# Optimization experiments

Measured on AMD Instinct MI355X. Metric: run time of the kernel, lower is better.

The kernel has to match this reference:

```python
import jax, jax.numpy as jnp
import numpy as np
import math

N_NODES = 50000
N_EDGES = 800000
NFEAT = 512
NHID = 128
NCLASS = 128
NLAYERS = 16
LAMDA = 0.5
ALPHA = 0.1


def setup_inputs() -> dict:
    key = jax.random.key(0)
    k1, k2, k3, k4, k5, k6, k7, k8 = jax.random.split(key, 8)
    x = jax.random.normal(k1, (N_NODES, NFEAT), dtype=jnp.float32)
    # edges with no self loops: col = (row + offset) % N, offset in [1, N)
    row = jax.random.randint(k2, (N_EDGES,), 0, N_NODES, dtype=jnp.int32)
    off = jax.random.randint(k3, (N_EDGES,), 1, N_NODES, dtype=jnp.int32)
    col = (row + off) % N_NODES
    edge_idx = jnp.stack([row, col], axis=0)
    # conv weights: uniform(-stdv, stdv), stdv = 1/sqrt(out_features)
    stdv = 1.0 / math.sqrt(NHID)
    conv_w = jax.random.uniform(k4, (NLAYERS, NHID, NHID), jnp.float32, -stdv, stdv)
    # fc layers (stored as [in, out]; equivalent to torch Linear y = x @ W.T + b)
    fc0_w = jax.random.normal(k5, (NFEAT, NHID), jnp.float32) * (1.0 / math.sqrt(NFEAT))
    fc0_b = jax.random.normal(k6, (NHID,), jnp.float32) * 0.01
    fc1_w = jax.random.normal(k7, (NHID, NCLASS), jnp.float32) * (1.0 / math.sqrt(NHID))
    fc1_b = jax.random.normal(k8, (NCLASS,), jnp.float32) * 0.01
    return {"x": x, "edge_idx": edge_idx, "conv_w": conv_w,
            "fc0_w": fc0_w, "fc0_b": fc0_b, "fc1_w": fc1_w, "fc1_b": fc1_b}


def reference(x, edge_idx, conv_w, fc0_w, fc0_b, fc1_w, fc1_b):
    # eval mode: dropout is identity
    n = x.shape[0]
    loop = jnp.arange(n, dtype=edge_idx.dtype)
    # add_remaining_self_loops: inputs have no self loops -> append unit loops
    row = jnp.concatenate([edge_idx[0], loop])
    col = jnp.concatenate([edge_idx[1], loop])
    w = jnp.ones(row.shape[0], dtype=x.dtype)
    # symmetric normalization: D^-1/2 A D^-1/2
    deg = jax.ops.segment_sum(w, row, num_segments=n)
    dinv = jnp.where(deg > 0, jax.lax.rsqrt(deg), 0.0).astype(x.dtype)
    w = dinv[row] * w * dinv[col]

    h0 = jax.nn.relu(x @ fc0_w + fc0_b)  # [N, NHID]
    thetas = jnp.log(LAMDA / jnp.arange(1, NLAYERS + 1, dtype=x.dtype) + 1.0)

    def layer(h, wt):
        Wl, theta = wt
        # SpMM: hi[r] = sum_{(r,c) in E} w_rc * h[c]
        hi = jax.ops.segment_sum(w[:, None] * h[col], row, num_segments=n)
        support = (1.0 - ALPHA) * hi + ALPHA * h0
        out = theta * (support @ Wl) + (1.0 - theta) * support
        return jax.nn.relu(out), None

    h, _ = jax.lax.scan(layer, h0, (conv_w, thetas))
    return h @ fc1_w + fc1_b  # [N, NCLASS]
```

## Files before the change

### kernel.cpp

```cpp
#include <hip/hip_runtime.h>
#include <hip/hip_bf16.h>
#include <math.h>

#define N_NODES_C 50000
#define N_EDGES_C 800000
#define NFEAT_C 512
#define NH_C 128
#define NLAYERS_C 16
#define LDB 136

typedef __attribute__((ext_vector_type(8))) short short8;
typedef __attribute__((ext_vector_type(4))) float f32x4;

__device__ __forceinline__ float b2f(unsigned short h) {
    union { unsigned int u; float f; } v; v.u = ((unsigned int)h) << 16; return v.f;
}
__device__ __forceinline__ unsigned short f2b(float f) {
    union { float f; unsigned int u; } v; v.f = f;
    unsigned int r = (v.u + 0x7fffu + ((v.u >> 16) & 1u)) >> 16;
    return (unsigned short)r;
}


__global__ __launch_bounds__(256) void k_count(const int* __restrict__ row,
                                               int* __restrict__ cnt) {
    int e = blockIdx.x * 256 + threadIdx.x;
    atomicAdd(&cnt[row[e]], 1);
}

__global__ __launch_bounds__(256) void k_scan1(const int* __restrict__ cnt,
                                               int* __restrict__ locex,
                                               int* __restrict__ partials, int n) {
    __shared__ int sm[256];
    int t = threadIdx.x;
    int i = blockIdx.x * 256 + t;
    int v = (i < n) ? cnt[i] : 0;
    sm[t] = v;
    __syncthreads();
    for (int o = 1; o < 256; o <<= 1) {
        int x = (t >= o) ? sm[t - o] : 0;
        __syncthreads();
        sm[t] += x;
        __syncthreads();
    }
    if (i < n) locex[i] = sm[t] - v;
    if (t == 255) partials[blockIdx.x] = sm[255];
}

__global__ __launch_bounds__(256) void k_scan2(int* __restrict__ partials, int np) {
    __shared__ int sm[256];
    int t = threadIdx.x;
    int v = (t < np) ? partials[t] : 0;
    sm[t] = v;
    __syncthreads();
    for (int o = 1; o < 256; o <<= 1) {
        int x = (t >= o) ? sm[t - o] : 0;
        __syncthreads();
        sm[t] += x;
        __syncthreads();
    }
    if (t < np) partials[t] = sm[t] - v;
}

__global__ __launch_bounds__(256) void k_scan3(const int* __restrict__ cnt,
                                               const int* __restrict__ locex,
                                               const int* __restrict__ partials,
                                               int* __restrict__ rowptr,
                                               int* __restrict__ cursor,
                                               float* __restrict__ dinv,
                                               int n, int ne) {
    int i = blockIdx.x * 256 + threadIdx.x;
    if (i < n) {
        int rp = locex[i] + partials[i >> 8];
        rowptr[i] = rp;
        cursor[i] = rp;
        dinv[i] = 1.0f / sqrtf((float)(cnt[i] + 1));
    }
    if (i == 0) rowptr[n] = ne;
}

__global__ __launch_bounds__(256) void k_fill(const int* __restrict__ row,
                                              const int* __restrict__ col,
                                              int* __restrict__ cursor,
                                              int* __restrict__ colsorted) {
    int e = blockIdx.x * 256 + threadIdx.x;
    int p = atomicAdd(&cursor[row[e]], 1);
    colsorted[p] = col[e];
}


__global__ __launch_bounds__(256) void k_convt128(const float* __restrict__ src,
                                                  unsigned short* __restrict__ dst,
                                                  int total) {
    int i = blockIdx.x * 256 + threadIdx.x;
    if (i >= total) return;
    int l = i >> 14, w = i & 16383;
    int n = w >> 7, k = w & 127;
    dst[i] = f2b(src[(l << 14) + (k << 7) + n]);
}

__global__ __launch_bounds__(256) void k_convt_fc0(const float* __restrict__ src,
                                                   unsigned short* __restrict__ dst) {
    int i = blockIdx.x * 256 + threadIdx.x;
    int n = i >> 9, k = i & 511;
    dst[i] = f2b(src[(k << 7) + n]);
}


__device__ __forceinline__ void acc8(float* a, uint4 u) {
    a[0] += b2f((unsigned short)(u.x & 0xffffu));
    a[1] += b2f((unsigned short)(u.x >> 16));
    a[2] += b2f((unsigned short)(u.y & 0xffffu));
    a[3] += b2f((unsigned short)(u.y >> 16));
    a[4] += b2f((unsigned short)(u.z & 0xffffu));
    a[5] += b2f((unsigned short)(u.z >> 16));
    a[6] += b2f((unsigned short)(u.w & 0xffffu));
    a[7] += b2f((unsigned short)(u.w >> 16));
}

__global__ __launch_bounds__(256) void k_spmm(const unsigned short* __restrict__ hs,
                                              const unsigned short* __restrict__ h0,
                                              const float* __restrict__ dinv,
                                              const int* __restrict__ rowptr,
                                              const int* __restrict__ cols,
                                              unsigned short* __restrict__ sout) {
    const int w = threadIdx.x >> 6, ln = threadIdx.x & 63;
    const int r = blockIdx.x * 4 + w;
    const int g = ln >> 4, gi = ln & 15;
    const uint4* hs4 = (const uint4*)hs;
    const uint4* h04 = (const uint4*)h0;

    float a[8];
#pragma unroll
    for (int j = 0; j < 8; j++) a[j] = 0.f;

    int e = rowptr[r];
    const int end = rowptr[r + 1];

    if (g == 0) {
        uint4 u = hs4[(size_t)r * 16 + gi];
        acc8(a, u);
    }
    for (; e + 15 < end; e += 16) {
        int cA = cols[e + g];
        int cB = cols[e + 4 + g];
        int cC = cols[e + 8 + g];
        int cD = cols[e + 12 + g];
        uint4 uA = hs4[(size_t)cA * 16 + gi];
        uint4 uB = hs4[(size_t)cB * 16 + gi];
        uint4 uC = hs4[(size_t)cC * 16 + gi];
        uint4 uD = hs4[(size_t)cD * 16 + gi];
        acc8(a, uA);
        acc8(a, uB);
        acc8(a, uC);
        acc8(a, uD);
    }
    for (; e + 3 < end; e += 4) {
        int c = cols[e + g];
        uint4 u = hs4[(size_t)c * 16 + gi];
        acc8(a, u);
    }
    int rem = end - e;
    if (g < rem) {
        int c = cols[e + g];
        uint4 u = hs4[(size_t)c * 16 + gi];
        acc8(a, u);
    }

#pragma unroll
    for (int j = 0; j < 8; j++) {
        a[j] += __shfl_xor(a[j], 16);
        a[j] += __shfl_xor(a[j], 32);
    }

    float dr = 0.9f * dinv[r];
    uint4 hv = h04[(size_t)r * 16 + gi];
    uint4 o;
    o.x = (unsigned int)f2b(dr * a[0] + 0.1f * b2f((unsigned short)(hv.x & 0xffffu))) |
          ((unsigned int)f2b(dr * a[1] + 0.1f * b2f((unsigned short)(hv.x >> 16))) << 16);
    o.y = (unsigned int)f2b(dr * a[2] + 0.1f * b2f((unsigned short)(hv.y & 0xffffu))) |
          ((unsigned int)f2b(dr * a[3] + 0.1f * b2f((unsigned short)(hv.y >> 16))) << 16);
    o.z = (unsigned int)f2b(dr * a[4] + 0.1f * b2f((unsigned short)(hv.z & 0xffffu))) |
          ((unsigned int)f2b(dr * a[5] + 0.1f * b2f((unsigned short)(hv.z >> 16))) << 16);
    o.w = (unsigned int)f2b(dr * a[6] + 0.1f * b2f((unsigned short)(hv.w & 0xffffu))) |
          ((unsigned int)f2b(dr * a[7] + 0.1f * b2f((unsigned short)(hv.w >> 16))) << 16);
    if (g == 0) ((uint4*)sout)[(size_t)r * 16 + gi] = o;
}


__global__ __launch_bounds__(256) void k_gemm_blend(
    const unsigned short* __restrict__ S, const float* __restrict__ dinv,
    const unsigned short* __restrict__ WT, unsigned short* __restrict__ hdst,
    float theta, int use_dinv) {
    __shared__ __align__(16) unsigned short s_lds[64 * LDB];
    __shared__ __align__(16) unsigned short bt[128 * LDB];
    const int tid = threadIdx.x;
    const int w = tid >> 6, ln = tid & 63;
    const int quad = ln >> 4, l16 = ln & 15;
    const int block_base = blockIdx.x * 64;

    for (int chunk = tid; chunk < 128 * 16; chunk += 256) {
        int n = chunk >> 4, k8 = (chunk & 15) << 3;
        *(short8*)&bt[n * LDB + k8] = *(const short8*)&WT[(n << 7) + k8];
    }
    for (int chunk = tid; chunk < 64 * 16; chunk += 256) {
        int n = chunk >> 4, k8 = (chunk & 15) << 3;
        int row = block_base + n;
        short8 v = {};
        if (row < N_NODES_C) v = *(const short8*)&S[(size_t)row * NH_C + k8];
        *(short8*)&s_lds[n * LDB + k8] = v;
    }
    __syncthreads();

    f32x4 acc[8];
#pragma unroll
    for (int j = 0; j < 8; j++) acc[j] = (f32x4){0.f, 0.f, 0.f, 0.f};
#pragma unroll
    for (int ki = 0; ki < 128; ki += 32) {
        short8 af = *(const short8*)&s_lds[((w << 4) + l16) * LDB + ki + quad * 8];
#pragma unroll
        for (int nt = 0; nt < 8; nt++) {
            short8 bf = *(const short8*)&bt[(nt * 16 + l16) * LDB + ki + quad * 8];
            acc[nt] = __builtin_amdgcn_mfma_f32_16x16x32_bf16(af, bf, acc[nt], 0, 0, 0);
        }
    }

#pragma unroll
    for (int reg = 0; reg < 4; reg++) {
        int lr = (w << 4) + (quad << 2) + reg;
        int r = block_base + lr;
        float drv = dinv[(r < N_NODES_C) ? r : (N_NODES_C - 1)];
#pragma unroll
        for (int nt = 0; nt < 8; nt++) {
            int n = nt * 16 + l16;
            float s = b2f(s_lds[lr * LDB + n]);
            float v = theta * acc[nt][reg] + (1.f - theta) * s;
            v = fmaxf(v, 0.f);
            if (use_dinv) v *= drv;
            s_lds[lr * LDB + n] = f2b(v);
        }
    }
#pragma unroll
    for (int it = 0; it < 4; it++) {
        int local = ln + it * 64;
        int lr = (w << 4) + (local >> 4);
        int c8 = (local & 15) << 3;
        int row = block_base + lr;
        if (row < N_NODES_C)
            *(short8*)&hdst[(size_t)row * NH_C + c8] = *(const short8*)&s_lds[lr * LDB + c8];
    }
}


template <int AFP32, int MT>
__global__ __launch_bounds__(256) void k_gemm(
    const void* __restrict__ Av, const unsigned short* __restrict__ WT,
    int M, int K,
    const float* __restrict__ bias, const float* __restrict__ dinv,
    unsigned short* __restrict__ out0, unsigned short* __restrict__ out1,
    float* __restrict__ outf, int mode) {
    __shared__ __align__(16) unsigned short bt[128 * LDB];
    const int tid = threadIdx.x;
    const int w = tid >> 6, ln = tid & 63;
    const int quad = ln >> 4, l16 = ln & 15;
    const int ROWS = 64 * MT;
    const int block_base = blockIdx.x * ROWS;
    const int m_base = block_base + w * (16 * MT);

    f32x4 acc[MT][8];
#pragma unroll
    for (int i = 0; i < MT; i++)
#pragma unroll
        for (int j = 0; j < 8; j++) acc[i][j] = (f32x4){0.f, 0.f, 0.f, 0.f};

    for (int kc = 0; kc < K; kc += 128) {
        float4 a_f[MT][4][2];
        short8 a_b[MT][4];
#pragma unroll
        for (int ki4 = 0; ki4 < 4; ki4++) {
#pragma unroll
            for (int mt = 0; mt < MT; mt++) {
                int row = m_base + mt * 16 + l16;
                if (row >= M) row = M - 1;
                if (AFP32) {
                    const float* A = (const float*)Av;
                    const float* p = &A[(size_t)row * K + kc + ki4 * 32 + quad * 8];
                    a_f[mt][ki4][0] = *(const float4*)p;
                    a_f[mt][ki4][1] = *(const float4*)(p + 4);
                } else {
                    const unsigned short* A = (const unsigned short*)Av;
                    a_b[mt][ki4] =
                        *(const short8*)&A[(size_t)row * K + kc + ki4 * 32 + quad * 8];
                }
            }
        }
        for (int chunk = tid; chunk < 128 * 16; chunk += 256) {
            int n = chunk >> 4, k8 = (chunk & 15) << 3;
            *(short8*)&bt[n * LDB + k8] = *(const short8*)&WT[(size_t)n * K + kc + k8];
        }
        __syncthreads();
#pragma unroll
        for (int ki4 = 0; ki4 < 4; ki4++) {
            short8 bf[8];
#pragma unroll
            for (int nt = 0; nt < 8; nt++)
                bf[nt] = *(const short8*)&bt[(nt * 16 + l16) * LDB + ki4 * 32 + quad * 8];
#pragma unroll
            for (int mt = 0; mt < MT; mt++) {
                short8 af;
                if (AFP32) {
                    float4 f0 = a_f[mt][ki4][0];
                    float4 f1 = a_f[mt][ki4][1];
                    af[0] = (short)f2b(f0.x); af[1] = (short)f2b(f0.y);
                    af[2] = (short)f2b(f0.z); af[3] = (short)f2b(f0.w);
                    af[4] = (short)f2b(f1.x); af[5] = (short)f2b(f1.y);
                    af[6] = (short)f2b(f1.z); af[7] = (short)f2b(f1.w);
                } else {
                    af = a_b[mt][ki4];
                }
#pragma unroll
                for (int nt = 0; nt < 8; nt++)
                    acc[mt][nt] = __builtin_amdgcn_mfma_f32_16x16x32_bf16(
                        af, bf[nt], acc[mt][nt], 0, 0, 0);
            }
        }
        __syncthreads();
    }

    if (mode == 2) {
#pragma unroll
        for (int mt = 0; mt < MT; mt++)
#pragma unroll
            for (int reg = 0; reg < 4; reg++) {
                int r = m_base + mt * 16 + quad * 4 + reg;
                if (r >= M) continue;
#pragma unroll
                for (int nt = 0; nt < 8; nt++) {
                    int n = nt * 16 + l16;
                    outf[(size_t)r * NH_C + n] = acc[mt][nt][reg] + bias[n];
                }
            }
        return;
    }

#pragma unroll
    for (int mt = 0; mt < MT; mt++)
#pragma unroll
        for (int reg = 0; reg < 4; reg++) {
            int lr = w * (16 * MT) + mt * 16 + quad * 4 + reg;
#pragma unroll
            for (int nt = 0; nt < 8; nt++) {
                int n = nt * 16 + l16;
                float v = acc[mt][nt][reg] + bias[n];
                bt[lr * LDB + n] = f2b(fmaxf(v, 0.f));
            }
        }
#pragma unroll
    for (int it = 0; it < 4 * MT; it++) {
        int local = ln + it * 64;
        int lr = w * (16 * MT) + (local >> 4);
        int c8 = (local & 15) << 3;
        int row = block_base + lr;
        if (row >= M) continue;
        short8 v = *(const short8*)&bt[lr * LDB + c8];
        *(short8*)&out1[(size_t)row * NH_C + c8] = v;
        float dr = dinv[row];
        short8 o;
#pragma unroll
        for (int j = 0; j < 8; j++)
            o[j] = (short)f2b(b2f((unsigned short)v[j]) * dr);
        *(short8*)&out0[(size_t)row * NH_C + c8] = o;
    }
}


extern "C" void kernel_launch(void* const* d_in, const int* in_sizes, int n_in,
                              void* d_out, int out_size, void* d_ws, size_t ws_size,
                              hipStream_t stream) {
    const float* x = (const float*)d_in[0];
    const int* edge = (const int*)d_in[1];
    const float* convw = (const float*)d_in[2];
    const float* fc0w = (const float*)d_in[3];
    const float* fc0b = (const float*)d_in[4];
    const float* fc1w = (const float*)d_in[5];
    const float* fc1b = (const float*)d_in[6];
    const int* erow = edge;
    const int* ecol = edge + N_EDGES_C;

    char* ws = (char*)d_ws;
    size_t off = 0;
    auto alloc = [&](size_t bytes) -> void* {
        off = (off + 255) & ~(size_t)255;
        void* p = ws + off;
        off += bytes;
        return p;
    };
    int* cnt = (int*)alloc(N_NODES_C * 4);
    int* cursor = (int*)alloc(N_NODES_C * 4);
    int* locex = (int*)alloc(N_NODES_C * 4);
    int* partials = (int*)alloc(1024);
    int* rowptr = (int*)alloc((N_NODES_C + 1) * 4);
    float* dinv = (float*)alloc(N_NODES_C * 4);
    int* colsorted = (int*)alloc(N_EDGES_C * 4);
    unsigned short* wconvT = (unsigned short*)alloc((size_t)NLAYERS_C * NH_C * NH_C * 2);
    unsigned short* wfc0T = (unsigned short*)alloc((size_t)NFEAT_C * NH_C * 2);
    unsigned short* wfc1T = (unsigned short*)alloc((size_t)NH_C * NH_C * 2);
    unsigned short* h0 = (unsigned short*)alloc((size_t)N_NODES_C * NH_C * 2);
    unsigned short* hsA = (unsigned short*)alloc((size_t)N_NODES_C * NH_C * 2);
    unsigned short* hsB = (unsigned short*)alloc((size_t)N_NODES_C * NH_C * 2);
    unsigned short* sbuf = (unsigned short*)alloc((size_t)N_NODES_C * NH_C * 2);
    (void)ws_size; (void)n_in; (void)in_sizes; (void)out_size;

    k_convt128<<<NLAYERS_C * NH_C * NH_C / 256, 256, 0, stream>>>(
        convw, wconvT, NLAYERS_C * NH_C * NH_C);
    k_convt_fc0<<<NFEAT_C * NH_C / 256, 256, 0, stream>>>(fc0w, wfc0T);
    k_convt128<<<NH_C * NH_C / 256, 256, 0, stream>>>(fc1w, wfc1T, NH_C * NH_C);

    hipMemsetAsync(cnt, 0, N_NODES_C * 4, stream);
    k_count<<<N_EDGES_C / 256, 256, 0, stream>>>(erow, cnt);
    const int NB = (N_NODES_C + 255) / 256;
    k_scan1<<<NB, 256, 0, stream>>>(cnt, locex, partials, N_NODES_C);
    k_scan2<<<1, 256, 0, stream>>>(partials, NB);
    k_scan3<<<NB, 256, 0, stream>>>(cnt, locex, partials, rowptr, cursor, dinv,
                                    N_NODES_C, N_EDGES_C);
    k_fill<<<N_EDGES_C / 256, 256, 0, stream>>>(erow, ecol, cursor, colsorted);

    const int GB1 = (N_NODES_C + 63) / 64;
    k_gemm<1, 1><<<GB1, 256, 0, stream>>>(x, wfc0T, N_NODES_C, NFEAT_C, fc0b, dinv,
                                          hsA, h0, nullptr, 0);
    unsigned short* cur = hsA;
    unsigned short* nxt = hsB;
    for (int l = 0; l < NLAYERS_C; l++) {
        k_spmm<<<N_NODES_C / 4, 256, 0, stream>>>(cur, h0, dinv, rowptr, colsorted,
                                                  sbuf);
        float theta = logf(0.5f / (float)(l + 1) + 1.0f);
        k_gemm_blend<<<GB1, 256, 0, stream>>>(sbuf, dinv,
                                              wconvT + (size_t)l * NH_C * NH_C, nxt,
                                              theta, (l < NLAYERS_C - 1) ? 1 : 0);
        unsigned short* t = cur; cur = nxt; nxt = t;
    }
    k_gemm<0, 1><<<GB1, 256, 0, stream>>>(cur, wfc1T, N_NODES_C, NH_C, fc1b, dinv,
                                          nullptr, nullptr, (float*)d_out, 2);
}
```

Measured before the change: 1.004 ms.

## Fuse SpMM aggregation into per-layer GEMM kernel via LDS

Merges the neighbor-aggregation SpMM and the dense blend GEMM into one kernel per layer. Each block gathers its 64 rows directly into shared memory, with each wave looping over 16 rows, and then runs the MFMA GEMM. This removes the intermediate support buffer round-trip through global memory and one launch per layer. In exchange it reduces gather parallelism: far fewer blocks, rows processed serially per wave, and high LDS use limiting occupancy.

```diff
diff --git a/kernel.cpp b/kernel.cpp
--- a/kernel.cpp
+++ b/kernel.cpp
@@ -118,99 +118,91 @@
     a[7] += b2f((unsigned short)(u.w >> 16));
 }
 
-__global__ __launch_bounds__(256) void k_spmm(const unsigned short* __restrict__ hs,
-                                              const unsigned short* __restrict__ h0,
-                                              const float* __restrict__ dinv,
-                                              const int* __restrict__ rowptr,
-                                              const int* __restrict__ cols,
-                                              unsigned short* __restrict__ sout) {
-    const int w = threadIdx.x >> 6, ln = threadIdx.x & 63;
-    const int r = blockIdx.x * 4 + w;
-    const int g = ln >> 4, gi = ln & 15;
-    const uint4* hs4 = (const uint4*)hs;
-    const uint4* h04 = (const uint4*)h0;
-
-    float a[8];
-#pragma unroll
-    for (int j = 0; j < 8; j++) a[j] = 0.f;
-
-    int e = rowptr[r];
-    const int end = rowptr[r + 1];
-
-    if (g == 0) {
-        uint4 u = hs4[(size_t)r * 16 + gi];
-        acc8(a, u);
-    }
-    for (; e + 15 < end; e += 16) {
-        int cA = cols[e + g];
-        int cB = cols[e + 4 + g];
-        int cC = cols[e + 8 + g];
-        int cD = cols[e + 12 + g];
-        uint4 uA = hs4[(size_t)cA * 16 + gi];
-        uint4 uB = hs4[(size_t)cB * 16 + gi];
-        uint4 uC = hs4[(size_t)cC * 16 + gi];
-        uint4 uD = hs4[(size_t)cD * 16 + gi];
-        acc8(a, uA);
-        acc8(a, uB);
-        acc8(a, uC);
-        acc8(a, uD);
-    }
-    for (; e + 3 < end; e += 4) {
-        int c = cols[e + g];
-        uint4 u = hs4[(size_t)c * 16 + gi];
-        acc8(a, u);
-    }
-    int rem = end - e;
-    if (g < rem) {
-        int c = cols[e + g];
-        uint4 u = hs4[(size_t)c * 16 + gi];
-        acc8(a, u);
-    }
-
-#pragma unroll
-    for (int j = 0; j < 8; j++) {
-        a[j] += __shfl_xor(a[j], 16);
-        a[j] += __shfl_xor(a[j], 32);
-    }
-
-    float dr = 0.9f * dinv[r];
-    uint4 hv = h04[(size_t)r * 16 + gi];
-    uint4 o;
-    o.x = (unsigned int)f2b(dr * a[0] + 0.1f * b2f((unsigned short)(hv.x & 0xffffu))) |
-          ((unsigned int)f2b(dr * a[1] + 0.1f * b2f((unsigned short)(hv.x >> 16))) << 16);
-    o.y = (unsigned int)f2b(dr * a[2] + 0.1f * b2f((unsigned short)(hv.y & 0xffffu))) |
-          ((unsigned int)f2b(dr * a[3] + 0.1f * b2f((unsigned short)(hv.y >> 16))) << 16);
-    o.z = (unsigned int)f2b(dr * a[4] + 0.1f * b2f((unsigned short)(hv.z & 0xffffu))) |
-          ((unsigned int)f2b(dr * a[5] + 0.1f * b2f((unsigned short)(hv.z >> 16))) << 16);
-    o.w = (unsigned int)f2b(dr * a[6] + 0.1f * b2f((unsigned short)(hv.w & 0xffffu))) |
-          ((unsigned int)f2b(dr * a[7] + 0.1f * b2f((unsigned short)(hv.w >> 16))) << 16);
-    if (g == 0) ((uint4*)sout)[(size_t)r * 16 + gi] = o;
-}
-
-
-__global__ __launch_bounds__(256) void k_gemm_blend(
-    const unsigned short* __restrict__ S, const float* __restrict__ dinv,
-    const unsigned short* __restrict__ WT, unsigned short* __restrict__ hdst,
-    float theta, int use_dinv) {
+__global__ __launch_bounds__(256) void k_layer(
+    const unsigned short* __restrict__ hs, const unsigned short* __restrict__ h0,
+    const float* __restrict__ dinv, const int* __restrict__ rowptr,
+    const int* __restrict__ cols, const unsigned short* __restrict__ WT,
+    unsigned short* __restrict__ hdst, float theta, int use_dinv) {
     __shared__ __align__(16) unsigned short s_lds[64 * LDB];
     __shared__ __align__(16) unsigned short bt[128 * LDB];
     const int tid = threadIdx.x;
     const int w = tid >> 6, ln = tid & 63;
     const int quad = ln >> 4, l16 = ln & 15;
+    const int g = ln >> 4, gi = ln & 15;
     const int block_base = blockIdx.x * 64;
+    const uint4* hs4 = (const uint4*)hs;
+    const uint4* h04 = (const uint4*)h0;
 
     for (int chunk = tid; chunk < 128 * 16; chunk += 256) {
         int n = chunk >> 4, k8 = (chunk & 15) << 3;
         *(short8*)&bt[n * LDB + k8] = *(const short8*)&WT[(n << 7) + k8];
     }
-    for (int chunk = tid; chunk < 64 * 16; chunk += 256) {
-        int n = chunk >> 4, k8 = (chunk & 15) << 3;
-        int row = block_base + n;
-        short8 v = {};
-        if (row < N_NODES_C) v = *(const short8*)&S[(size_t)row * NH_C + k8];
-        *(short8*)&s_lds[n * LDB + k8] = v;
-    }
     __syncthreads();
+
+    for (int i = 0; i < 16; i++) {
+        const int lr = (w << 4) + i;
+        const int r = block_base + lr;
+        if (r >= N_NODES_C) {
+            if (g == 0) {
+                uint4 z = {0u, 0u, 0u, 0u};
+                *(uint4*)&s_lds[lr * LDB + (gi << 3)] = z;
+            }
+            continue;
+        }
+        float a[8];
+#pragma unroll
+        for (int j = 0; j < 8; j++) a[j] = 0.f;
+        int e = rowptr[r];
+        const int end = rowptr[r + 1];
+        if (g == 0) {
+            uint4 u = hs4[(size_t)r * 16 + gi];
+            acc8(a, u);
+        }
+        for (; e + 15 < end; e += 16) {
+            int cA = cols[e + g];
+            int cB = cols[e + 4 + g];
+            int cC = cols[e + 8 + g];
+            int cD = cols[e + 12 + g];
+            uint4 uA = hs4[(size_t)cA * 16 + gi];
+            uint4 uB = hs4[(size_t)cB * 16 + gi];
+            uint4 uC = hs4[(size_t)cC * 16 + gi];
+            uint4 uD = hs4[(size_t)cD * 16 + gi];
+            acc8(a, uA);
+            acc8(a, uB);
+            acc8(a, uC);
+            acc8(a, uD);
+        }
+        for (; e + 3 < end; e += 4) {
+            int c = cols[e + g];
+            uint4 u = hs4[(size_t)c * 16 + gi];
+            acc8(a, u);
+        }
+        int rem = end - e;
+        if (g < rem) {
+            int c = cols[e + g];
+            uint4 u = hs4[(size_t)c * 16 + gi];
+            acc8(a, u);
+        }
+#pragma unroll
+        for (int j = 0; j < 8; j++) {
+            a[j] += __shfl_xor(a[j], 16);
+            a[j] += __shfl_xor(a[j], 32);
+        }
+        if (g == 0) {
+            float dr = 0.9f * dinv[r];
+            uint4 hv = h04[(size_t)r * 16 + gi];
+            uint4 o;
+            o.x = (unsigned int)f2b(dr * a[0] + 0.1f * b2f((unsigned short)(hv.x & 0xffffu))) |
+                  ((unsigned int)f2b(dr * a[1] + 0.1f * b2f((unsigned short)(hv.x >> 16))) << 16);
+            o.y = (unsigned int)f2b(dr * a[2] + 0.1f * b2f((unsigned short)(hv.y & 0xffffu))) |
+                  ((unsigned int)f2b(dr * a[3] + 0.1f * b2f((unsigned short)(hv.y >> 16))) << 16);
+            o.z = (unsigned int)f2b(dr * a[4] + 0.1f * b2f((unsigned short)(hv.z & 0xffffu))) |
+                  ((unsigned int)f2b(dr * a[5] + 0.1f * b2f((unsigned short)(hv.z >> 16))) << 16);
+            o.w = (unsigned int)f2b(dr * a[6] + 0.1f * b2f((unsigned short)(hv.w & 0xffffu))) |
+                  ((unsigned int)f2b(dr * a[7] + 0.1f * b2f((unsigned short)(hv.w >> 16))) << 16);
+            *(uint4*)&s_lds[lr * LDB + (gi << 3)] = o;
+        }
+    }
 
     f32x4 acc[8];
 #pragma unroll
@@ -408,7 +400,6 @@
     unsigned short* h0 = (unsigned short*)alloc((size_t)N_NODES_C * NH_C * 2);
     unsigned short* hsA = (unsigned short*)alloc((size_t)N_NODES_C * NH_C * 2);
     unsigned short* hsB = (unsigned short*)alloc((size_t)N_NODES_C * NH_C * 2);
-    unsigned short* sbuf = (unsigned short*)alloc((size_t)N_NODES_C * NH_C * 2);
     (void)ws_size; (void)n_in; (void)in_sizes; (void)out_size;
 
     k_convt128<<<NLAYERS_C * NH_C * NH_C / 256, 256, 0, stream>>>(
@@ -431,12 +422,10 @@
     unsigned short* cur = hsA;
     unsigned short* nxt = hsB;
     for (int l = 0; l < NLAYERS_C; l++) {
-        k_spmm<<<N_NODES_C / 4, 256, 0, stream>>>(cur, h0, dinv, rowptr, colsorted,
-                                                  sbuf);
         float theta = logf(0.5f / (float)(l + 1) + 1.0f);
-        k_gemm_blend<<<GB1, 256, 0, stream>>>(sbuf, dinv,
-                                              wconvT + (size_t)l * NH_C * NH_C, nxt,
-                                              theta, (l < NLAYERS_C - 1) ? 1 : 0);
+        k_layer<<<GB1, 256, 0, stream>>>(cur, h0, dinv, rowptr, colsorted,
+                                         wconvT + (size_t)l * NH_C * NH_C, nxt,
+                                         theta, (l < NLAYERS_C - 1) ? 1 : 0);
         unsigned short* t = cur; cur = nxt; nxt = t;
     }
     k_gemm<0, 1><<<GB1, 256, 0, stream>>>(cur, wfc1T, N_NODES_C, NH_C, fc1b, dinv,
```

Result: slower. 1.793 ms (+78.5%).
